# Kernel optimization log

Measured on AMD Instinct MI355X. Metric: run time of the kernel, lower is better.

Reference implementation:

```python
import jax, jax.numpy as jnp
import numpy as np

N_ATOMS = 100_000
N_PAIRS = 3_200_000


def setup_inputs() -> dict:
    key = jax.random.key(0)
    k0, k1, k2, k3, k4 = jax.random.split(key, 5)
    atomic_numbers = jax.random.randint(k0, (N_ATOMS,), 1, 95, dtype=jnp.int32)
    distances = jax.random.uniform(k1, (N_PAIRS,), jnp.float32, 0.5, 5.0)
    cutoffs = jax.random.uniform(k2, (N_PAIRS,), jnp.float32)
    idx_i = jnp.sort(jax.random.randint(k3, (N_PAIRS,), 0, N_ATOMS, dtype=jnp.int32))
    idx_j = jax.random.randint(k4, (N_PAIRS,), 0, N_ATOMS, dtype=jnp.int32)
    # ZBL parameters (trainable=True defaults from __init__)
    a_coefficient = jnp.array([0.8854], dtype=jnp.float32)
    a_exponent = jnp.array([0.23], dtype=jnp.float32)
    phi_coefficients = jnp.array([0.18175, 0.50986, 0.28022, 0.02817], dtype=jnp.float32)
    phi_exponents = jnp.array([3.1998, 0.94229, 0.4029, 0.20162], dtype=jnp.float32)
    # unit conversion buffers: identity units -> factors = 1.0
    ke = jnp.array([1.0 / (4.0 * np.pi * 0.005526349406)], dtype=jnp.float32)
    distances_model2Ang = jnp.array([1.0], dtype=jnp.float32)
    energies_Hatree2model = jnp.array([1.0], dtype=jnp.float32)
    return dict(atomic_numbers=atomic_numbers, distances=distances, cutoffs=cutoffs,
                idx_i=idx_i, idx_j=idx_j, a_coefficient=a_coefficient,
                a_exponent=a_exponent, phi_coefficients=phi_coefficients,
                phi_exponents=phi_exponents, ke=ke,
                distances_model2Ang=distances_model2Ang,
                energies_Hatree2model=energies_Hatree2model)


def reference(atomic_numbers, distances, cutoffs, idx_i, idx_j,
              a_coefficient, a_exponent, phi_coefficients, phi_exponents,
              ke, distances_model2Ang, energies_Hatree2model):
    Z = atomic_numbers.astype(distances.dtype)            # [N]
    distances_ang = distances * distances_model2Ang        # [P]
    za = Z ** jnp.abs(a_exponent)                          # [N] (a_exponent is [1])
    a_ij = jnp.abs(a_coefficient) / (za[idx_i] + za[idx_j])  # [P]
    arguments = distances / a_ij                           # [P] (faithful: uses model-unit distances)
    # L1-normalized |phi_coefficients|
    abs_c = jnp.abs(phi_coefficients)
    coefficients = abs_c / jnp.sum(abs_c)                  # [4]
    exponents = jnp.abs(phi_exponents)                     # [4]
    # phi[p] = sum_k c_k * exp(-e_k * arg_p)  -> [P,4] intermediate
    phi = jnp.sum(coefficients[None, :] * jnp.exp(-exponents[None, :] * arguments[:, None]), axis=1)
    repulsion = ke * Z[idx_i] * Z[idx_j] / distances_ang * phi * cutoffs  # [P]
    Erep = energies_Hatree2model * jax.ops.segment_sum(repulsion, idx_i, num_segments=N_ATOMS)
    return Erep
```

## Files before the change

### kernel.cpp

```cpp
#include <hip/hip_runtime.h>
#include <hip/hip_bf16.h>
#include <math.h>

#define LOG2E 1.4426950408889634f

__global__ void zbl_precompute_za(const int* __restrict__ Z,
                                  const float* __restrict__ a_exp,
                                  float2* __restrict__ zfza, int n) {
    int i = blockIdx.x * blockDim.x + threadIdx.x;
    if (i < n) {
        float zf = (float)Z[i];
        float za = powf(zf, fabsf(a_exp[0]));
        zfza[i] = make_float2(zf, za);
    }
}

__global__ void __launch_bounds__(256)
zbl_pairs(const float* __restrict__ dist, const float* __restrict__ cut,
          const int* __restrict__ idx_i, const int* __restrict__ idx_j,
          const float2* __restrict__ zfza,
          const float* __restrict__ a_coef,
          const float* __restrict__ phi_c, const float* __restrict__ phi_e,
          const float* __restrict__ ke, const float* __restrict__ d2a,
          const float* __restrict__ e2m,
          float* __restrict__ out, int n) {
    float inv_ac = __fdividef(1.0f, fabsf(a_coef[0]));
    float c0 = fabsf(phi_c[0]), c1 = fabsf(phi_c[1]),
          c2 = fabsf(phi_c[2]), c3 = fabsf(phi_c[3]);
    float cnorm = __fdividef(1.0f, c0 + c1 + c2 + c3);
    c0 *= cnorm; c1 *= cnorm; c2 *= cnorm; c3 *= cnorm;
    float e0 = fabsf(phi_e[0]) * LOG2E, e1 = fabsf(phi_e[1]) * LOG2E,
          e2 = fabsf(phi_e[2]) * LOG2E, e3 = fabsf(phi_e[3]) * LOG2E;
    float scale = ke[0] * e2m[0];
    float d2a0  = d2a[0];

    int p = blockIdx.x * blockDim.x + threadIdx.x;

    int   ii  = -1;
    float val = 0.0f;
    if (p < n) {
        ii = idx_i[p];
        int jj = idx_j[p];
        float2 zi = zfza[ii];
        float2 zj = zfza[jj];
        float d   = dist[p];
        float arg = d * (zi.y + zj.y) * inv_ac;
        float phi = c0 * exp2f(-e0 * arg) + c1 * exp2f(-e1 * arg)
                  + c2 * exp2f(-e2 * arg) + c3 * exp2f(-e3 * arg);
        val = scale * zi.x * zj.x * phi * cut[p];
        val = __fdividef(val, d * d2a0);
    }

    int lane = threadIdx.x & 63;
    #pragma unroll
    for (int off = 1; off < 64; off <<= 1) {
        float ov = __shfl_up(val, (unsigned)off, 64);
        int   oi = __shfl_up(ii, (unsigned)off, 64);
        if (lane >= off && oi == ii) val += ov;
    }
    int nxt = __shfl_down(ii, 1u, 64);
    bool tail = (lane == 63) || (nxt != ii);
    if (p < n && tail) atomicAdd(out + ii, val);
}

__global__ void __launch_bounds__(256)
zbl_pairs_nows(const float* __restrict__ dist, const float* __restrict__ cut,
               const int* __restrict__ idx_i, const int* __restrict__ idx_j,
               const int* __restrict__ Z,
               const float* __restrict__ a_coef, const float* __restrict__ a_exp,
               const float* __restrict__ phi_c, const float* __restrict__ phi_e,
               const float* __restrict__ ke, const float* __restrict__ d2a,
               const float* __restrict__ e2m,
               float* __restrict__ out, int n) {
    float inv_ac = __fdividef(1.0f, fabsf(a_coef[0]));
    float aexp = fabsf(a_exp[0]);
    float c0 = fabsf(phi_c[0]), c1 = fabsf(phi_c[1]),
          c2 = fabsf(phi_c[2]), c3 = fabsf(phi_c[3]);
    float cnorm = __fdividef(1.0f, c0 + c1 + c2 + c3);
    c0 *= cnorm; c1 *= cnorm; c2 *= cnorm; c3 *= cnorm;
    float e0 = fabsf(phi_e[0]) * LOG2E, e1 = fabsf(phi_e[1]) * LOG2E,
          e2 = fabsf(phi_e[2]) * LOG2E, e3 = fabsf(phi_e[3]) * LOG2E;
    float scale = ke[0] * e2m[0];
    float d2a0  = d2a[0];

    int p = blockIdx.x * blockDim.x + threadIdx.x;
    int   ii  = -1;
    float val = 0.0f;
    if (p < n) {
        ii = idx_i[p];
        int jj = idx_j[p];
        float zif = (float)Z[ii];
        float zjf = (float)Z[jj];
        float zai = exp2f(__log2f(zif) * aexp);
        float zaj = exp2f(__log2f(zjf) * aexp);
        float d   = dist[p];
        float arg = d * (zai + zaj) * inv_ac;
        float phi = c0 * exp2f(-e0 * arg) + c1 * exp2f(-e1 * arg)
                  + c2 * exp2f(-e2 * arg) + c3 * exp2f(-e3 * arg);
        val = scale * zif * zjf * phi * cut[p];
        val = __fdividef(val, d * d2a0);
    }

    int lane = threadIdx.x & 63;
    #pragma unroll
    for (int off = 1; off < 64; off <<= 1) {
        float ov = __shfl_up(val, (unsigned)off, 64);
        int   oi = __shfl_up(ii, (unsigned)off, 64);
        if (lane >= off && oi == ii) val += ov;
    }
    int nxt = __shfl_down(ii, 1u, 64);
    bool tail = (lane == 63) || (nxt != ii);
    if (p < n && tail) atomicAdd(out + ii, val);
}

extern "C" void kernel_launch(void* const* d_in, const int* in_sizes, int n_in,
                              void* d_out, int out_size, void* d_ws, size_t ws_size,
                              hipStream_t stream) {
    const int*   atomic_numbers = (const int*)  d_in[0];
    const float* distances      = (const float*)d_in[1];
    const float* cutoffs        = (const float*)d_in[2];
    const int*   idx_i          = (const int*)  d_in[3];
    const int*   idx_j          = (const int*)  d_in[4];
    const float* a_coefficient  = (const float*)d_in[5];
    const float* a_exponent     = (const float*)d_in[6];
    const float* phi_coeffs     = (const float*)d_in[7];
    const float* phi_exps       = (const float*)d_in[8];
    const float* ke             = (const float*)d_in[9];
    const float* d2a            = (const float*)d_in[10];
    const float* e2m            = (const float*)d_in[11];
    float* out = (float*)d_out;

    const int n_atoms = in_sizes[0];
    const int n_pairs = in_sizes[1];

    hipMemsetAsync(d_out, 0, (size_t)out_size * sizeof(float), stream);

    const int block = 256;
    const int grid_pairs = (n_pairs + block - 1) / block;

    size_t need = (size_t)n_atoms * sizeof(float2);
    if (ws_size >= need) {
        float2* zfza = (float2*)d_ws;
        int grid_atoms = (n_atoms + block - 1) / block;
        zbl_precompute_za<<<grid_atoms, block, 0, stream>>>(
            atomic_numbers, a_exponent, zfza, n_atoms);
        zbl_pairs<<<grid_pairs, block, 0, stream>>>(
            distances, cutoffs, idx_i, idx_j, zfza,
            a_coefficient, phi_coeffs, phi_exps, ke, d2a, e2m,
            out, n_pairs);
    } else {
        zbl_pairs_nows<<<grid_pairs, block, 0, stream>>>(
            distances, cutoffs, idx_i, idx_j, atomic_numbers,
            a_coefficient, a_exponent, phi_coeffs, phi_exps, ke, d2a, e2m,
            out, n_pairs);
    }
}
```

Measured before the change: 123.1 us.

## Compress atomic numbers to bytes, use shared za lookup table, fuse output zeroing

```diff
diff --git a/kernel.cpp b/kernel.cpp
--- a/kernel.cpp
+++ b/kernel.cpp
@@ -4,26 +4,27 @@
 
 #define LOG2E 1.4426950408889634f
 
-__global__ void zbl_precompute_za(const int* __restrict__ Z,
-                                  const float* __restrict__ a_exp,
-                                  float2* __restrict__ zfza, int n) {
+__global__ void __launch_bounds__(256)
+zbl_prep(const int* __restrict__ Z, unsigned char* __restrict__ z8,
+         float* __restrict__ out, int n_atoms, int out_n) {
     int i = blockIdx.x * blockDim.x + threadIdx.x;
-    if (i < n) {
-        float zf = (float)Z[i];
-        float za = powf(zf, fabsf(a_exp[0]));
-        zfza[i] = make_float2(zf, za);
-    }
+    if (i < n_atoms) z8[i] = (unsigned char)Z[i];
+    if (i < out_n)   out[i] = 0.0f;
 }
 
+template <typename ZT>
 __global__ void __launch_bounds__(256)
 zbl_pairs(const float* __restrict__ dist, const float* __restrict__ cut,
           const int* __restrict__ idx_i, const int* __restrict__ idx_j,
-          const float2* __restrict__ zfza,
-          const float* __restrict__ a_coef,
+          const ZT* __restrict__ zt,
+          const float* __restrict__ a_coef, const float* __restrict__ a_exp,
           const float* __restrict__ phi_c, const float* __restrict__ phi_e,
           const float* __restrict__ ke, const float* __restrict__ d2a,
           const float* __restrict__ e2m,
           float* __restrict__ out, int n) {
+    __shared__ float za_tab[128];
+
+    float aexp   = fabsf(a_exp[0]);
     float inv_ac = __fdividef(1.0f, fabsf(a_coef[0]));
     float c0 = fabsf(phi_c[0]), c1 = fabsf(phi_c[1]),
           c2 = fabsf(phi_c[2]), c3 = fabsf(phi_c[3]);
@@ -32,76 +33,31 @@
     float e0 = fabsf(phi_e[0]) * LOG2E, e1 = fabsf(phi_e[1]) * LOG2E,
           e2 = fabsf(phi_e[2]) * LOG2E, e3 = fabsf(phi_e[3]) * LOG2E;
     float scale = ke[0] * e2m[0];
-    float d2a0  = d2a[0];
+    float inv_d2a = __fdividef(1.0f, d2a[0]);
 
-    int p = blockIdx.x * blockDim.x + threadIdx.x;
+    int t = threadIdx.x;
+    if (t < 128) za_tab[t] = powf((float)t, aexp);
+    __syncthreads();
+
+    int p = blockIdx.x * blockDim.x + t;
 
     int   ii  = -1;
     float val = 0.0f;
     if (p < n) {
         ii = idx_i[p];
         int jj = idx_j[p];
-        float2 zi = zfza[ii];
-        float2 zj = zfza[jj];
+        int zi = (int)zt[ii];
+        int zj = (int)zt[jj];
+        float zif = (float)zi, zjf = (float)zj;
         float d   = dist[p];
-        float arg = d * (zi.y + zj.y) * inv_ac;
+        float arg = d * (za_tab[zi] + za_tab[zj]) * inv_ac;
         float phi = c0 * exp2f(-e0 * arg) + c1 * exp2f(-e1 * arg)
                   + c2 * exp2f(-e2 * arg) + c3 * exp2f(-e3 * arg);
-        val = scale * zi.x * zj.x * phi * cut[p];
-        val = __fdividef(val, d * d2a0);
+        float invd = __fdividef(1.0f, d);
+        val = scale * zif * zjf * phi * cut[p] * invd * inv_d2a;
     }
 
-    int lane = threadIdx.x & 63;
-    #pragma unroll
-    for (int off = 1; off < 64; off <<= 1) {
-        float ov = __shfl_up(val, (unsigned)off, 64);
-        int   oi = __shfl_up(ii, (unsigned)off, 64);
-        if (lane >= off && oi == ii) val += ov;
-    }
-    int nxt = __shfl_down(ii, 1u, 64);
-    bool tail = (lane == 63) || (nxt != ii);
-    if (p < n && tail) atomicAdd(out + ii, val);
-}
-
-__global__ void __launch_bounds__(256)
-zbl_pairs_nows(const float* __restrict__ dist, const float* __restrict__ cut,
-               const int* __restrict__ idx_i, const int* __restrict__ idx_j,
-               const int* __restrict__ Z,
-               const float* __restrict__ a_coef, const float* __restrict__ a_exp,
-               const float* __restrict__ phi_c, const float* __restrict__ phi_e,
-               const float* __restrict__ ke, const float* __restrict__ d2a,
-               const float* __restrict__ e2m,
-               float* __restrict__ out, int n) {
-    float inv_ac = __fdividef(1.0f, fabsf(a_coef[0]));
-    float aexp = fabsf(a_exp[0]);
-    float c0 = fabsf(phi_c[0]), c1 = fabsf(phi_c[1]),
-          c2 = fabsf(phi_c[2]), c3 = fabsf(phi_c[3]);
-    float cnorm = __fdividef(1.0f, c0 + c1 + c2 + c3);
-    c0 *= cnorm; c1 *= cnorm; c2 *= cnorm; c3 *= cnorm;
-    float e0 = fabsf(phi_e[0]) * LOG2E, e1 = fabsf(phi_e[1]) * LOG2E,
-          e2 = fabsf(phi_e[2]) * LOG2E, e3 = fabsf(phi_e[3]) * LOG2E;
-    float scale = ke[0] * e2m[0];
-    float d2a0  = d2a[0];
-
-    int p = blockIdx.x * blockDim.x + threadIdx.x;
-    int   ii  = -1;
-    float val = 0.0f;
-    if (p < n) {
-        ii = idx_i[p];
-        int jj = idx_j[p];
-        float zif = (float)Z[ii];
-        float zjf = (float)Z[jj];
-        float zai = exp2f(__log2f(zif) * aexp);
-        float zaj = exp2f(__log2f(zjf) * aexp);
-        float d   = dist[p];
-        float arg = d * (zai + zaj) * inv_ac;
-        float phi = c0 * exp2f(-e0 * arg) + c1 * exp2f(-e1 * arg)
-                  + c2 * exp2f(-e2 * arg) + c3 * exp2f(-e3 * arg);
-        val = scale * zif * zjf * phi * cut[p];
-        val = __fdividef(val, d * d2a0);
-    }
-
-    int lane = threadIdx.x & 63;
+    int lane = t & 63;
     #pragma unroll
     for (int off = 1; off < 64; off <<= 1) {
         float ov = __shfl_up(val, (unsigned)off, 64);
@@ -133,23 +89,21 @@
     const int n_atoms = in_sizes[0];
     const int n_pairs = in_sizes[1];
 
-    hipMemsetAsync(d_out, 0, (size_t)out_size * sizeof(float), stream);
-
     const int block = 256;
     const int grid_pairs = (n_pairs + block - 1) / block;
+    const int grid_prep  = (((n_atoms > out_size) ? n_atoms : out_size) + block - 1) / block;
 
-    size_t need = (size_t)n_atoms * sizeof(float2);
-    if (ws_size >= need) {
-        float2* zfza = (float2*)d_ws;
-        int grid_atoms = (n_atoms + block - 1) / block;
-        zbl_precompute_za<<<grid_atoms, block, 0, stream>>>(
-            atomic_numbers, a_exponent, zfza, n_atoms);
-        zbl_pairs<<<grid_pairs, block, 0, stream>>>(
-            distances, cutoffs, idx_i, idx_j, zfza,
-            a_coefficient, phi_coeffs, phi_exps, ke, d2a, e2m,
+    if (ws_size >= (size_t)n_atoms) {
+        unsigned char* z8 = (unsigned char*)d_ws;
+        zbl_prep<<<grid_prep, block, 0, stream>>>(
+            atomic_numbers, z8, out, n_atoms, out_size);
+        zbl_pairs<unsigned char><<<grid_pairs, block, 0, stream>>>(
+            distances, cutoffs, idx_i, idx_j, z8,
+            a_coefficient, a_exponent, phi_coeffs, phi_exps, ke, d2a, e2m,
             out, n_pairs);
     } else {
-        zbl_pairs_nows<<<grid_pairs, block, 0, stream>>>(
+        hipMemsetAsync(d_out, 0, (size_t)out_size * sizeof(float), stream);
+        zbl_pairs<int><<<grid_pairs, block, 0, stream>>>(
             distances, cutoffs, idx_i, idx_j, atomic_numbers,
             a_coefficient, a_exponent, phi_coeffs, phi_exps, ke, d2a, e2m,
             out, n_pairs);
```

Result: slower. 127.4 us (+3.5%).
